# Kernel optimization log

Hardware: AMD Instinct MI355X
Metric: run time of the kernel (lower is better)

Reference implementation:

```python
import jax, jax.numpy as jnp
import numpy as np

S, H, I, E, TOP_K = 8192, 2048, 2048, 8, 2


def setup_inputs() -> dict:
    key = jax.random.key(0)
    k0, k1, k2, k3 = jax.random.split(key, 4)
    scale = 1.0 / np.sqrt(H)
    return {
        "hidden_states": jax.random.normal(k0, (S, H), dtype=jnp.float32),
        "w_gate": jax.random.normal(k1, (E, H), dtype=jnp.float32) * scale,
        "w1": jax.random.normal(k2, (E, 2 * I, H), dtype=jnp.float32) * scale,
        "w2": jax.random.normal(k3, (E, H, I), dtype=jnp.float32) * (1.0 / np.sqrt(I)),
        "top_k": TOP_K,
    }


def reference(hidden_states, w_gate, w1, w2, top_k):
    # Router: logits -> float32 softmax -> top-k -> renormalize
    router_logits = hidden_states @ w_gate.T                      # [S, E]
    probs = jax.nn.softmax(router_logits.astype(jnp.float32), axis=-1)
    top_p, top_i = jax.lax.top_k(probs, top_k)                    # [S, k]
    top_p = top_p / jnp.sum(top_p, axis=-1, keepdims=True)

    n_tok, n_exp = probs.shape
    # Dense combine weights [S, E]; zero for non-selected experts.
    combine = jnp.zeros((n_tok, n_exp), dtype=probs.dtype)
    combine = combine.at[jnp.arange(n_tok)[:, None], top_i].add(top_p)

    inter = w2.shape[2]
    out = jnp.zeros_like(hidden_states)
    # Loop over the small fixed expert set; masked-combine gives exact
    # fused_moe semantics (scatter-combine of weighted expert outputs).
    for e in range(n_exp):
        gu = hidden_states @ w1[e].T                              # [S, 2I]
        gate, up = gu[:, :inter], gu[:, inter:]
        h = jax.nn.silu(gate) * up                                # SiluAndMul
        out = out + combine[:, e:e + 1].astype(hidden_states.dtype) * (h @ w2[e].T)
    return out, router_logits
```

## Files before the change

### kernel.cpp

```cpp
#include <hip/hip_runtime.h>
#include <hip/hip_bf16.h>
#include <stdint.h>

#define S_TOK 8192
#define H_DIM 2048
#define I_DIM 2048
#define E_NUM 8

typedef __attribute__((ext_vector_type(4))) float f32x4;
typedef __attribute__((ext_vector_type(8))) short bf16x8;
typedef __attribute__((ext_vector_type(8))) unsigned short u16x8;

#define MFMA16(a, b, c) __builtin_amdgcn_mfma_f32_16x16x32_bf16((a), (b), (c), 0, 0, 0)

__device__ __forceinline__ unsigned short f2bf(float f) {
    unsigned int u = __float_as_uint(f);
    unsigned int r = (u + 0x7FFFu + ((u >> 16) & 1u)) >> 16;
    return (unsigned short)r;
}
__device__ __forceinline__ float bf2f(unsigned short u) {
    return __uint_as_float((unsigned int)u << 16);
}

__device__ __forceinline__ void cvt8(const float* __restrict__ s, unsigned short* __restrict__ d) {
    float4 v0 = *(const float4*)s;
    float4 v1 = *(const float4*)(s + 4);
    u16x8 o;
    o[0] = f2bf(v0.x); o[1] = f2bf(v0.y); o[2] = f2bf(v0.z); o[3] = f2bf(v0.w);
    o[4] = f2bf(v1.x); o[5] = f2bf(v1.y); o[6] = f2bf(v1.z); o[7] = f2bf(v1.w);
    *(u16x8*)d = o;
}

__device__ __forceinline__ void async_copy16(void* lds, const void* g) {
    __builtin_amdgcn_global_load_lds(
        (const __attribute__((address_space(1))) void*)(uintptr_t)g,
        (__attribute__((address_space(3))) void*)(uintptr_t)lds,
        16, 0, 0);
}

__device__ __forceinline__ int xcd_swizzle(int bid, int nwg) {
    int cpx = nwg >> 3;
    return (bid & 7) * cpx + (bid >> 3);
}

__global__ void cvt_kernel(const float* __restrict__ src, unsigned short* __restrict__ dst, long n) {
    long i0 = ((long)blockIdx.x * blockDim.x + threadIdx.x) * 8;
    long stride = (long)gridDim.x * blockDim.x * 8;
    for (long i = i0; i < n; i += stride) cvt8(src + i, dst + i);
}

template<int HALF>
__device__ __forceinline__ void cvt_w1_half_body(const float* __restrict__ src,
                                                 unsigned short* __restrict__ dst,
                                                 long i0, long stride) {
    const long CH = 1L << 21;
    const long TOT = (long)E_NUM * 2 * CH;
    for (long j = i0; j < TOT; j += stride) {
        long e = j >> 22;
        long piece = (j >> 21) & 1;
        long off = j & (CH - 1);
        long g = (e << 23) + ((piece * 2 + HALF) << 21) + off;
        cvt8(src + g, dst + g);
    }
}

template<int HALF>
__global__ void cvt_w1_half_kernel(const float* __restrict__ src, unsigned short* __restrict__ dst) {
    long i0 = ((long)blockIdx.x * blockDim.x + threadIdx.x) * 8;
    long stride = (long)gridDim.x * blockDim.x * 8;
    cvt_w1_half_body<HALF>(src, dst, i0, stride);
}

__global__ void router_kernel(const float* __restrict__ hs, const float* __restrict__ wg,
                              float* __restrict__ logits, int* __restrict__ cnt,
                              int* __restrict__ tok_of, float* __restrict__ wgt_of,
                              unsigned int* __restrict__ slot_of,
                              unsigned short* __restrict__ hsb) {
    int t = blockIdx.x;
    int tid = threadIdx.x;
    const float* hrow = hs + (size_t)t * H_DIM;
    float4 h0 = *(const float4*)(hrow + tid * 8);
    float4 h1 = *(const float4*)(hrow + tid * 8 + 4);
    u16x8 o;
    o[0] = f2bf(h0.x); o[1] = f2bf(h0.y); o[2] = f2bf(h0.z); o[3] = f2bf(h0.w);
    o[4] = f2bf(h1.x); o[5] = f2bf(h1.y); o[6] = f2bf(h1.z); o[7] = f2bf(h1.w);
    *(u16x8*)(hsb + (size_t)t * H_DIM + tid * 8) = o;

    float p[E_NUM];
#pragma unroll
    for (int e = 0; e < E_NUM; ++e) {
        const float* w = wg + (size_t)e * H_DIM + tid * 8;
        float4 w0 = *(const float4*)(w);
        float4 w1v = *(const float4*)(w + 4);
        p[e] = h0.x * w0.x + h0.y * w0.y + h0.z * w0.z + h0.w * w0.w +
               h1.x * w1v.x + h1.y * w1v.y + h1.z * w1v.z + h1.w * w1v.w;
    }
#pragma unroll
    for (int e = 0; e < E_NUM; ++e)
#pragma unroll
        for (int d = 32; d > 0; d >>= 1) p[e] += __shfl_xor(p[e], d, 64);

    __shared__ float red[4][E_NUM];
    int wave = tid >> 6, lane = tid & 63;
    if (lane == 0) {
#pragma unroll
        for (int e = 0; e < E_NUM; ++e) red[wave][e] = p[e];
    }
    __syncthreads();
    if (tid == 0) {
        float l[E_NUM];
#pragma unroll
        for (int e = 0; e < E_NUM; ++e) l[e] = red[0][e] + red[1][e] + red[2][e] + red[3][e];
#pragma unroll
        for (int e = 0; e < E_NUM; ++e) logits[(size_t)t * E_NUM + e] = l[e];
        int i1 = 0;
#pragma unroll
        for (int e = 1; e < E_NUM; ++e) if (l[e] > l[i1]) i1 = e;
        int i2 = (i1 == 0) ? 1 : 0;
#pragma unroll
        for (int e = 0; e < E_NUM; ++e) if (e != i1 && l[e] > l[i2]) i2 = e;
        float b = __expf(l[i2] - l[i1]);
        float wA = 1.0f / (1.0f + b);
        float wB = 1.0f - wA;
        int s1 = atomicAdd(&cnt[i1], 1);
        tok_of[i1 * S_TOK + s1] = t; wgt_of[i1 * S_TOK + s1] = wA;
        int s2 = atomicAdd(&cnt[i2], 1);
        tok_of[i2 * S_TOK + s2] = t; wgt_of[i2 * S_TOK + s2] = wB;
        slot_of[2 * t]     = ((unsigned)i1 << 20) | (unsigned)s1;
        slot_of[2 * t + 1] = ((unsigned)i2 << 20) | (unsigned)s2;
    }
}

__global__ void offsets_kernel(const int* __restrict__ cnt, int* __restrict__ off) {
    if (threadIdx.x == 0) {
        int s = 0;
        for (int e = 0; e < E_NUM; ++e) { off[e] = s; s += cnt[e]; }
    }
}

__global__ void combine_kernel(const unsigned short* __restrict__ pbuf,
                               const unsigned int* __restrict__ slot_of,
                               const int* __restrict__ off, float* __restrict__ out) {
    int t = blockIdx.x, tid = threadIdx.x;
    unsigned int a = slot_of[2 * t], b = slot_of[2 * t + 1];
    size_t ra = (size_t)(off[a >> 20] + (int)(a & 0xFFFFFu));
    size_t rb = (size_t)(off[b >> 20] + (int)(b & 0xFFFFFu));
    const unsigned short* pa = pbuf + ra * H_DIM + tid * 8;
    const unsigned short* pb = pbuf + rb * H_DIM + tid * 8;
    ushort4 a0 = *(const ushort4*)pa, a1 = *(const ushort4*)(pa + 4);
    ushort4 b0 = *(const ushort4*)pb, b1 = *(const ushort4*)(pb + 4);
    float4 r0, r1;
    r0.x = bf2f(a0.x) + bf2f(b0.x); r0.y = bf2f(a0.y) + bf2f(b0.y);
    r0.z = bf2f(a0.z) + bf2f(b0.z); r0.w = bf2f(a0.w) + bf2f(b0.w);
    r1.x = bf2f(a1.x) + bf2f(b1.x); r1.y = bf2f(a1.y) + bf2f(b1.y);
    r1.z = bf2f(a1.z) + bf2f(b1.z); r1.w = bf2f(a1.w) + bf2f(b1.w);
    float* op = out + (size_t)t * H_DIM + tid * 8;
    *(float4*)op = r0;
    *(float4*)(op + 4) = r1;
}

template<int IS_G1>
__global__ __launch_bounds__(512, 2) void moe_gemm_kernel(
    const unsigned short* __restrict__ A_src, const unsigned short* __restrict__ W,
    const int* __restrict__ cnt, const int* __restrict__ off,
    const int* __restrict__ tok_of, const float* __restrict__ wgt_of,
    unsigned short* __restrict__ dst,
    const float* __restrict__ cvt_src, unsigned short* __restrict__ cvt_dst,
    long cvt_n, int gemm_grid, int cvt_blks, int nt_base, int cvt_mode) {
    if ((int)blockIdx.x >= gemm_grid) {
        long i0 = ((long)((int)blockIdx.x - gemm_grid) * blockDim.x + threadIdx.x) * 8;
        long stride = (long)cvt_blks * blockDim.x * 8;
        if (cvt_mode == 2) {
            cvt_w1_half_body<1>(cvt_src, cvt_dst, i0, stride);
        } else {
            for (long i = i0; i < cvt_n; i += stride) cvt8(cvt_src + i, cvt_dst + i);
        }
        return;
    }
    int bx = xcd_swizzle(blockIdx.x, gemm_grid);
    int nt = nt_base + bx / (E_NUM * 32);
    int rr = bx % (E_NUM * 32);
    int e = rr / 32;
    int mt = rr % 32;
    int C = cnt[e];
    if (mt * 256 >= C) return;
    int O = off[e];

    __shared__ __align__(16) char ldsA[2][32768];
    __shared__ __align__(16) char ldsB[2][32768];

    int tid = threadIdx.x;
    int wave = tid >> 6, lane = tid & 63;
    int wr = wave >> 2, wc = wave & 3;

    const char* aptr[4];
#pragma unroll
    for (int q = 0; q < 4; ++q) {
        int row = q * 64 + wave * 8 + (lane >> 3);
        int cu = (lane & 7) ^ (row & 7);
        int grow = mt * 256 + row; if (grow > C - 1) grow = C - 1;
        size_t arow = IS_G1 ? (size_t)tok_of[e * S_TOK + grow] : (size_t)(O + grow);
        aptr[q] = (const char*)(A_src + arow * 2048 + cu * 8);
    }
    const char* bptr[4];
#pragma unroll
    for (int j = 0; j < 4; ++j) {
        int lrow = j * 64 + wave * 8 + (lane >> 3);
        int cu = (lane & 7) ^ (lrow & 7);
        int np = lrow >> 7, wcg = (lrow >> 5) & 3, rem = lrow & 31;
        int tbrow = wcg * 64 + np * 32 + rem;
        size_t brow;
        if (IS_G1) {
            int jj = tbrow & 63, wq = tbrow >> 6;
            if (jj < 32) brow = (size_t)(nt * 128 + wq * 32 + jj);
            else         brow = (size_t)I_DIM + nt * 128 + wq * 32 + (jj - 32);
            brow += (size_t)e * (2 * I_DIM);
        } else {
            brow = (size_t)e * H_DIM + nt * 256 + tbrow;
        }
        bptr[j] = (const char*)(W + brow * 2048 + cu * 8);
    }

    int aoff[8][2], boff[4][2];
#pragma unroll
    for (int m = 0; m < 8; ++m)
#pragma unroll
        for (int ks = 0; ks < 2; ++ks) {
            int row = wr * 128 + m * 16 + (lane & 15);
            int cu = ks * 4 + (lane >> 4);
            aoff[m][ks] = row * 128 + ((cu ^ (row & 7)) * 16);
        }
#pragma unroll
    for (int n = 0; n < 4; ++n)
#pragma unroll
        for (int ks = 0; ks < 2; ++ks) {
            int lrow = (n >> 1) * 128 + wc * 32 + (n & 1) * 16 + (lane & 15);
            int cu = ks * 4 + (lane >> 4);
            boff[n][ks] = lrow * 128 + ((cu ^ (lrow & 7)) * 16);
        }

    f32x4 acc[8][4];
#pragma unroll
    for (int m = 0; m < 8; ++m)
#pragma unroll
        for (int n = 0; n < 4; ++n)
#pragma unroll
            for (int q = 0; q < 4; ++q) acc[m][n][q] = 0.0f;

    auto gA = [&](int q, int T, int buf) {
        async_copy16(ldsA[buf] + q * 8192 + wave * 1024, aptr[q] + T * 128);
    };
    auto gB = [&](int j, int T, int buf) {
        async_copy16(ldsB[buf] + j * 8192 + wave * 1024, bptr[j] + T * 128);
    };

    gA(0, 0, 0); gA(2, 0, 0); gA(1, 0, 0); gA(3, 0, 0);
    gB(0, 0, 0); gB(1, 0, 0);
    gA(0, 1, 1); gA(2, 1, 1); gA(1, 1, 1); gA(3, 1, 1);
    gB(2, 0, 0); gB(3, 0, 0);
    asm volatile("s_waitcnt vmcnt(6)" ::: "memory");
    __builtin_amdgcn_s_barrier();

    bf16x8 ar[8][2], br[2][2];
    int cur = 0;
#pragma unroll 2
    for (int T = 0; T < 32; ++T) {
        int nxt = cur ^ 1;
        int TA = (T + 2 < 32) ? T + 2 : 31;
        int TB = (T + 1 < 32) ? T + 1 : 31;
#pragma unroll
        for (int n = 0; n < 2; ++n)
#pragma unroll
            for (int ks = 0; ks < 2; ++ks)
                br[n][ks] = *(const bf16x8*)(ldsB[cur] + boff[n][ks]);
#pragma unroll
        for (int m = 0; m < 4; ++m)
#pragma unroll
            for (int ks = 0; ks < 2; ++ks)
                ar[m][ks] = *(const bf16x8*)(ldsA[cur] + aoff[m][ks]);
        gB(0, TB, nxt); gB(1, TB, nxt);
        __builtin_amdgcn_s_setprio(1);
#pragma unroll
        for (int m = 0; m < 4; ++m)
#pragma unroll
            for (int n = 0; n < 2; ++n) {
                acc[m][n] = MFMA16(ar[m][0], br[n][0], acc[m][n]);
                acc[m][n] = MFMA16(ar[m][1], br[n][1], acc[m][n]);
            }
        __builtin_amdgcn_s_setprio(0);
        __builtin_amdgcn_s_barrier();
#pragma unroll
        for (int m = 4; m < 8; ++m)
#pragma unroll
            for (int ks = 0; ks < 2; ++ks)
                ar[m][ks] = *(const bf16x8*)(ldsA[cur] + aoff[m][ks]);
        gA(0, TA, cur); gA(2, TA, cur);
        __builtin_amdgcn_s_setprio(1);
#pragma unroll
        for (int m = 4; m < 8; ++m)
#pragma unroll
            for (int n = 0; n < 2; ++n) {
                acc[m][n] = MFMA16(ar[m][0], br[n][0], acc[m][n]);
                acc[m][n] = MFMA16(ar[m][1], br[n][1], acc[m][n]);
            }
        __builtin_amdgcn_s_setprio(0);
        asm volatile("s_waitcnt vmcnt(4)" ::: "memory");
        __builtin_amdgcn_s_barrier();
#pragma unroll
        for (int n = 0; n < 2; ++n)
#pragma unroll
            for (int ks = 0; ks < 2; ++ks)
                br[n][ks] = *(const bf16x8*)(ldsB[cur] + boff[n + 2][ks]);
        gA(1, TA, cur); gA(3, TA, cur);
        __builtin_amdgcn_s_setprio(1);
#pragma unroll
        for (int m = 0; m < 4; ++m)
#pragma unroll
            for (int n = 0; n < 2; ++n) {
                acc[m][n + 2] = MFMA16(ar[m][0], br[n][0], acc[m][n + 2]);
                acc[m][n + 2] = MFMA16(ar[m][1], br[n][1], acc[m][n + 2]);
            }
        __builtin_amdgcn_s_setprio(0);
        __builtin_amdgcn_s_barrier();
        gB(2, TB, nxt); gB(3, TB, nxt);
        __builtin_amdgcn_s_setprio(1);
#pragma unroll
        for (int m = 4; m < 8; ++m)
#pragma unroll
            for (int n = 0; n < 2; ++n) {
                acc[m][n + 2] = MFMA16(ar[m][0], br[n][0], acc[m][n + 2]);
                acc[m][n + 2] = MFMA16(ar[m][1], br[n][1], acc[m][n + 2]);
            }
        __builtin_amdgcn_s_setprio(0);
        asm volatile("s_waitcnt vmcnt(6)" ::: "memory");
        __builtin_amdgcn_s_barrier();
        cur = nxt;
    }

    if (IS_G1) {
#pragma unroll
        for (int m = 0; m < 8; ++m)
#pragma unroll
            for (int q = 0; q < 4; ++q) {
                int row = mt * 256 + wr * 128 + m * 16 + (lane >> 4) * 4 + q;
                if (row < C) {
                    float wgt = wgt_of[e * S_TOK + row];
                    unsigned short* hp = dst + (size_t)(O + row) * I_DIM +
                                         nt * 128 + wc * 32 + (lane & 15);
#pragma unroll
                    for (int n = 0; n < 2; ++n) {
                        float g = acc[m][n][q];
                        float u = acc[m][n + 2][q];
                        float hv = (g / (1.0f + __expf(-g))) * u * wgt;
                        hp[n * 16] = f2bf(hv);
                    }
                }
            }
    } else {
#pragma unroll
        for (int m = 0; m < 8; ++m)
#pragma unroll
            for (int q = 0; q < 4; ++q) {
                int row = mt * 256 + wr * 128 + m * 16 + (lane >> 4) * 4 + q;
                if (row < C) {
                    unsigned short* pp = dst + (size_t)(O + row) * H_DIM +
                                         nt * 256 + wc * 64 + (lane & 15);
#pragma unroll
                    for (int n = 0; n < 4; ++n)
                        pp[n * 16] = f2bf(acc[m][n][q]);
                }
            }
    }
}

extern "C" void kernel_launch(void* const* d_in, const int* in_sizes, int n_in,
                              void* d_out, int out_size, void* d_ws, size_t ws_size,
                              hipStream_t stream) {
    const float* hs = (const float*)d_in[0];
    const float* wg = (const float*)d_in[1];
    const float* w1 = (const float*)d_in[2];
    const float* w2 = (const float*)d_in[3];

    float* out = (float*)d_out;
    float* logits = out + (size_t)S_TOK * H_DIM;

    char* ws = (char*)d_ws;
    int* cnt = (int*)ws;
    int* off = (int*)(ws + 256);
    int* tok_of = (int*)(ws + 512);
    float* wgt_of = (float*)(ws + 512 + (size_t)E_NUM * S_TOK * 4);
    unsigned int* slot_of = (unsigned int*)(ws + 512 + (size_t)E_NUM * S_TOK * 8);
    size_t o = 512 + (size_t)E_NUM * S_TOK * 8 + (size_t)S_TOK * 8;
    o = (o + 4095) & ~(size_t)4095;
    unsigned short* hsb = (unsigned short*)(ws + o);  o += (size_t)S_TOK * H_DIM * 2;
    unsigned short* wxb = (unsigned short*)(ws + o);  o += (size_t)E_NUM * 2 * I_DIM * H_DIM * 2;
    unsigned short* hbuf = (unsigned short*)(ws + o); o += (size_t)S_TOK * 2 * I_DIM * 2;
    size_t o_w2 = o;
    size_t need_fused = o_w2 + (size_t)E_NUM * H_DIM * I_DIM * 2;
    bool fused = (ws_size >= need_fused);

    const long W1_N = (long)E_NUM * 2 * I_DIM * H_DIM;
    const long W2_N = (long)E_NUM * H_DIM * I_DIM;
    const int G1H_GRID = E_NUM * 32 * 8;
    const int G2_GRID = E_NUM * 32 * 8;
    const int CVT_BLKS = 1024;

    hipMemsetAsync(cnt, 0, 64, stream);
    router_kernel<<<S_TOK, 256, 0, stream>>>(hs, wg, logits, cnt, tok_of, wgt_of, slot_of, hsb);
    offsets_kernel<<<1, 64, 0, stream>>>(cnt, off);

    if (fused) {
        unsigned short* w2b = (unsigned short*)(ws + o_w2);
        unsigned short* pbuf = wxb;
        cvt_w1_half_kernel<0><<<4096, 256, 0, stream>>>(w1, wxb);
        moe_gemm_kernel<1><<<G1H_GRID + CVT_BLKS, 512, 0, stream>>>(
            hsb, wxb, cnt, off, tok_of, wgt_of, hbuf,
            w1, wxb, 0, G1H_GRID, CVT_BLKS, 0, 2);
        moe_gemm_kernel<1><<<G1H_GRID + CVT_BLKS, 512, 0, stream>>>(
            hsb, wxb, cnt, off, tok_of, wgt_of, hbuf,
            w2, w2b, W2_N, G1H_GRID, CVT_BLKS, 8, 1);
        moe_gemm_kernel<0><<<G2_GRID, 512, 0, stream>>>(
            hbuf, w2b, cnt, off, tok_of, wgt_of, pbuf,
            nullptr, nullptr, 0, G2_GRID, 0, 0, 0);
        combine_kernel<<<S_TOK, 256, 0, stream>>>(pbuf, slot_of, off, out);
    } else {
        unsigned short* w2b = wxb;
        unsigned short* pbuf = wxb + (size_t)E_NUM * H_DIM * I_DIM;
        cvt_kernel<<<4096, 256, 0, stream>>>(w1, wxb, W1_N);
        moe_gemm_kernel<1><<<E_NUM * 32 * 16, 512, 0, stream>>>(
            hsb, wxb, cnt, off, tok_of, wgt_of, hbuf,
            nullptr, nullptr, 0, E_NUM * 32 * 16, 0, 0, 0);
        cvt_kernel<<<4096, 256, 0, stream>>>(w2, w2b, W2_N);
        moe_gemm_kernel<0><<<G2_GRID, 512, 0, stream>>>(
            hbuf, w2b, cnt, off, tok_of, wgt_of, pbuf,
            nullptr, nullptr, 0, G2_GRID, 0, 0, 0);
        combine_kernel<<<S_TOK, 256, 0, stream>>>(pbuf, slot_of, off, out);
    }
}
```

Before: 738.7 us.

## Replace atomic expert slot assignment with deterministic single-block prefix scan

The router no longer does atomicAdd per token to claim expert slots; it writes each token's top-2 choice and weight to a buffer. A new single-block 1024-thread scan kernel counts per-expert tokens, computes exclusive prefix sums in shared memory, and writes tok_of/wgt_of/slot_of in token order. This removes the memset, the offsets kernel and contention on global atomics, and produces token-ordered expert lists that may improve locality in the gathers. The cost is a serial single-block kernel on the critical path.

```diff
diff --git a/kernel.cpp b/kernel.cpp
--- a/kernel.cpp
+++ b/kernel.cpp
@@ -72,9 +72,8 @@
 }
 
 __global__ void router_kernel(const float* __restrict__ hs, const float* __restrict__ wg,
-                              float* __restrict__ logits, int* __restrict__ cnt,
-                              int* __restrict__ tok_of, float* __restrict__ wgt_of,
-                              unsigned int* __restrict__ slot_of,
+                              float* __restrict__ logits,
+                              unsigned int* __restrict__ tchoice, float* __restrict__ twgt,
                               unsigned short* __restrict__ hsb) {
     int t = blockIdx.x;
     int tid = threadIdx.x;
@@ -120,21 +119,68 @@
 #pragma unroll
         for (int e = 0; e < E_NUM; ++e) if (e != i1 && l[e] > l[i2]) i2 = e;
         float b = __expf(l[i2] - l[i1]);
-        float wA = 1.0f / (1.0f + b);
-        float wB = 1.0f - wA;
-        int s1 = atomicAdd(&cnt[i1], 1);
+        tchoice[t] = (unsigned)i1 | ((unsigned)i2 << 4);
+        twgt[t] = 1.0f / (1.0f + b);
+    }
+}
+
+__global__ __launch_bounds__(1024) void scan_kernel(
+    const unsigned int* __restrict__ tchoice, const float* __restrict__ twgt,
+    int* __restrict__ cnt, int* __restrict__ off,
+    int* __restrict__ tok_of, float* __restrict__ wgt_of,
+    unsigned int* __restrict__ slot_of) {
+    __shared__ int lcnt[E_NUM][1024];
+    __shared__ int tot[E_NUM];
+    int tid = threadIdx.x;
+    unsigned int ch[8];
+    int c[E_NUM];
+#pragma unroll
+    for (int e = 0; e < E_NUM; ++e) c[e] = 0;
+#pragma unroll
+    for (int k = 0; k < 8; ++k) {
+        ch[k] = tchoice[tid * 8 + k];
+        c[ch[k] & 15]++;
+        c[(ch[k] >> 4) & 15]++;
+    }
+#pragma unroll
+    for (int e = 0; e < E_NUM; ++e) lcnt[e][tid] = c[e];
+    __syncthreads();
+    int wave = tid >> 6, lane = tid & 63;
+    if (wave < E_NUM) {
+        int base = 0;
+        for (int chk = 0; chk < 16; ++chk) {
+            int v = lcnt[wave][chk * 64 + lane];
+            int inc = v;
+#pragma unroll
+            for (int d = 1; d < 64; d <<= 1) {
+                int u = __shfl_up(inc, d, 64);
+                if (lane >= d) inc += u;
+            }
+            lcnt[wave][chk * 64 + lane] = base + inc - v;
+            base += __shfl(inc, 63, 64);
+        }
+        if (lane == 0) tot[wave] = base;
+    }
+    __syncthreads();
+    if (tid == 0) {
+        int s = 0;
+#pragma unroll
+        for (int e = 0; e < E_NUM; ++e) { off[e] = s; cnt[e] = tot[e]; s += tot[e]; }
+    }
+    __syncthreads();
+#pragma unroll
+    for (int e = 0; e < E_NUM; ++e) c[e] = lcnt[e][tid];
+#pragma unroll
+    for (int k = 0; k < 8; ++k) {
+        int t = tid * 8 + k;
+        int i1 = ch[k] & 15, i2 = (ch[k] >> 4) & 15;
+        float wA = twgt[t];
+        int s1 = c[i1]++;
+        int s2 = c[i2]++;
         tok_of[i1 * S_TOK + s1] = t; wgt_of[i1 * S_TOK + s1] = wA;
-        int s2 = atomicAdd(&cnt[i2], 1);
-        tok_of[i2 * S_TOK + s2] = t; wgt_of[i2 * S_TOK + s2] = wB;
+        tok_of[i2 * S_TOK + s2] = t; wgt_of[i2 * S_TOK + s2] = 1.0f - wA;
         slot_of[2 * t]     = ((unsigned)i1 << 20) | (unsigned)s1;
         slot_of[2 * t + 1] = ((unsigned)i2 << 20) | (unsigned)s2;
-    }
-}
-
-__global__ void offsets_kernel(const int* __restrict__ cnt, int* __restrict__ off) {
-    if (threadIdx.x == 0) {
-        int s = 0;
-        for (int e = 0; e < E_NUM; ++e) { off[e] = s; s += cnt[e]; }
     }
 }
 
@@ -390,7 +436,9 @@
     int* tok_of = (int*)(ws + 512);
     float* wgt_of = (float*)(ws + 512 + (size_t)E_NUM * S_TOK * 4);
     unsigned int* slot_of = (unsigned int*)(ws + 512 + (size_t)E_NUM * S_TOK * 8);
-    size_t o = 512 + (size_t)E_NUM * S_TOK * 8 + (size_t)S_TOK * 8;
+    unsigned int* tchoice = (unsigned int*)(ws + 512 + (size_t)E_NUM * S_TOK * 8 + (size_t)S_TOK * 8);
+    float* twgt = (float*)(ws + 512 + (size_t)E_NUM * S_TOK * 8 + (size_t)S_TOK * 12);
+    size_t o = 512 + (size_t)E_NUM * S_TOK * 8 + (size_t)S_TOK * 16;
     o = (o + 4095) & ~(size_t)4095;
     unsigned short* hsb = (unsigned short*)(ws + o);  o += (size_t)S_TOK * H_DIM * 2;
     unsigned short* wxb = (unsigned short*)(ws + o);  o += (size_t)E_NUM * 2 * I_DIM * H_DIM * 2;
@@ -405,9 +453,8 @@
     const int G2_GRID = E_NUM * 32 * 8;
     const int CVT_BLKS = 1024;
 
-    hipMemsetAsync(cnt, 0, 64, stream);
-    router_kernel<<<S_TOK, 256, 0, stream>>>(hs, wg, logits, cnt, tok_of, wgt_of, slot_of, hsb);
-    offsets_kernel<<<1, 64, 0, stream>>>(cnt, off);
+    router_kernel<<<S_TOK, 256, 0, stream>>>(hs, wg, logits, tchoice, twgt, hsb);
+    scan_kernel<<<1, 1024, 0, stream>>>(tchoice, twgt, cnt, off, tok_of, wgt_of, slot_of);
 
     if (fused) {
         unsigned short* w2b = (unsigned short*)(ws + o_w2);
```

After: 607.3 us. -17.8%, faster.
